# Optimization experiments

Hardware: AMD Instinct MI355X
Metric: run time of the kernel (lower is better)

## Reference

```python
import jax, jax.numpy as jnp
import numpy as np

NB_CLASSES = 10
EPS = 1e-8  # torch cosine_similarity eps


def gcn_conv(x, W, b, src, dst, n):
    h = x @ W
    deg = jax.ops.segment_sum(jnp.ones_like(src, dtype=h.dtype), dst, num_segments=n) + 1.0
    dinv = deg ** -0.5
    coef = (dinv[src] * dinv[dst])[:, None]
    agg = jax.ops.segment_sum(h[src] * coef, dst, num_segments=n)
    return agg + h * (1.0 / deg)[:, None] + b


def condition_net(e, w_in, b_in, w_hid, b_hid, w_out, b_out):
    # ConditionNet with num_layers=2: input_fc -> elu -> hidden_fc[0] -> elu -> output_fc
    h = jax.nn.elu(e @ w_in + b_in)
    h = jax.nn.elu(h @ w_hid + b_hid)
    return h @ w_out + b_out


def setup_inputs() -> dict:
    key = jax.random.key(0)
    N, E, D, H, T, M = 20000, 320000, 256, 256, 3, 2048
    ks = jax.random.split(key, 24)
    s = 1.0 / np.sqrt(D)
    inp = {
        "x": jax.random.normal(ks[0], (N, D), dtype=jnp.float32),
        "src": jax.random.randint(ks[1], (E,), 0, N, dtype=jnp.int32),
        "dst": jax.random.randint(ks[2], (E,), 0, N, dtype=jnp.int32),
        "idx": jax.random.randint(ks[3], (M,), 0, N, dtype=jnp.int32),
        "labels": jax.random.randint(ks[4], (M,), 0, NB_CLASSES, dtype=jnp.int32),
        "train": 1,
        # 3 GCNConv layers (all D->D, residual structure forces equal widths)
        "gcn_W1": jax.random.normal(ks[5], (D, D), dtype=jnp.float32) * s,
        "gcn_b1": jnp.zeros((D,), dtype=jnp.float32),
        "gcn_W2": jax.random.normal(ks[6], (D, D), dtype=jnp.float32) * s,
        "gcn_b2": jnp.zeros((D,), dtype=jnp.float32),
        "gcn_W3": jax.random.normal(ks[7], (D, D), dtype=jnp.float32) * s,
        "gcn_b3": jnp.zeros((D,), dtype=jnp.float32),
        # T=3 ConditionNets, params stacked on leading axis
        "cn_w_in": jax.random.normal(ks[8], (T, D, H), dtype=jnp.float32) * s,
        "cn_b_in": jnp.zeros((T, H), dtype=jnp.float32),
        "cn_w_hid": jax.random.normal(ks[9], (T, H, H), dtype=jnp.float32) * s,
        "cn_b_hid": jnp.zeros((T, H), dtype=jnp.float32),
        "cn_w_out": jax.random.normal(ks[10], (T, H, D), dtype=jnp.float32) * s,
        "cn_b_out": jnp.zeros((T, D), dtype=jnp.float32),
        # Embed_prompt
        "p_list": jax.random.normal(ks[11], (5, D), dtype=jnp.float32) * s,
        "a_W": jax.random.normal(ks[12], (D, 5), dtype=jnp.float32) * s,
        "a_b": jnp.zeros((5,), dtype=jnp.float32),
        # gcn_weight2 (trainable); weight1 and weight3 are frozen zeros, closed over
        "gcn_weight2": jnp.float32(1.0),
    }
    return inp


def reference(x, src, dst, idx, labels, train,
              gcn_W1, gcn_b1, gcn_W2, gcn_b2, gcn_W3, gcn_b3,
              cn_w_in, cn_b_in, cn_w_hid, cn_b_hid, cn_w_out, cn_b_out,
              p_list, a_W, a_b, gcn_weight2):
    n = x.shape[0]
    origin_x = x
    w1 = jnp.float32(0.0)  # gcn_weight1 (frozen)
    w3 = jnp.float32(0.0)  # gcn_weight3 (frozen)
    T = cn_w_in.shape[0]
    for t in range(T):  # think layers (small static count)
        e1 = gcn_conv(x, gcn_W1, gcn_b1, src, dst, n)
        e2 = gcn_conv(e1, gcn_W2, gcn_b2, src, dst, n) + e1
        e3 = gcn_conv(e2, gcn_W3, gcn_b3, src, dst, n) + e2
        embed = w1 * e1 + gcn_weight2 * e2 + w3 * e3
        prompt = condition_net(embed, cn_w_in[t], cn_b_in[t], cn_w_hid[t], cn_b_hid[t],
                               cn_w_out[t], cn_b_out[t])
        x = prompt * origin_x
    # full gcn(x, edge_index): 3 convs with ELU activation (standard GCN forward)
    h = jax.nn.elu(gcn_conv(x, gcn_W1, gcn_b1, src, dst, n))
    h = jax.nn.elu(gcn_conv(h, gcn_W2, gcn_b2, src, dst, n))
    h = jax.nn.elu(gcn_conv(h, gcn_W3, gcn_b3, src, dst, n))
    # Embed_prompt: attention over 5 learned prompt vectors
    weight = jax.nn.softmax(h @ a_W + a_b, axis=1)  # [N, 5]
    embed = h + weight @ p_list
    rawret = embed[idx]  # [M, D]
    # train==1: class prototypes via scatter-mean over labels
    sums = jax.ops.segment_sum(rawret, labels, num_segments=NB_CLASSES)
    counts = jax.ops.segment_sum(jnp.ones_like(labels, dtype=rawret.dtype), labels,
                                 num_segments=NB_CLASSES)
    ave = sums / jnp.maximum(counts, 1.0)[:, None]  # [C, D]
    # fused cosine similarity: normalize both, one matmul (replaces M*C scalar loop)
    rn = rawret / jnp.maximum(jnp.linalg.norm(rawret, axis=1, keepdims=True), EPS)
    an = ave / jnp.maximum(jnp.linalg.norm(ave, axis=1, keepdims=True), EPS)
    ret = jax.nn.softmax(rn @ an.T, axis=1)  # [M, C]
    return ret
```

## Files before the change

kernel.cpp:

```cpp
#include <hip/hip_runtime.h>
#include <hip/hip_bf16.h>
#include <math.h>

#define NN 20000
#define DD 256
#define EE 320000
#define MM 2048
#define CC 10
#define TT 3

typedef __attribute__((ext_vector_type(8))) short s8v;
typedef __attribute__((ext_vector_type(4))) float f4v;

__device__ unsigned short g_xb[NN * DD];
__device__ unsigned short g_xo[NN * DD];
__device__ unsigned short g_hb[NN * DD];
__device__ unsigned short g_e1b[NN * DD];
__device__ unsigned short g_e2b[NN * DD];
__device__ int   g_cnt[NN];
__device__ int   g_cursor[NN];
__device__ int   g_rowstart[NN + 1];
__device__ float g_dinv[NN];
__device__ float g_invdeg[NN];
__device__ int   g_part[128];
__device__ int2  g_edge[EE];
__device__ float g_sums[CC * DD];
__device__ float g_cntf[CC];
__device__ unsigned short g_wT1[12 * DD * DD];
__device__ unsigned short g_wT2[12 * DD * DD];

__device__ __forceinline__ float wave_sum(float v) {
#pragma unroll
  for (int off = 32; off > 0; off >>= 1) v += __shfl_xor(v, off);
  return v;
}

__device__ __forceinline__ float eluf(float x) {
  return x > 0.f ? x : expm1f(x);
}

__device__ __forceinline__ float2 bfpair(unsigned int d) {
  union { unsigned int i; float f; } a, b;
  a.i = d << 16;
  b.i = d & 0xffff0000u;
  return make_float2(a.f, b.f);
}

__device__ __forceinline__ unsigned int packbf(float x, float y) {
  union { __hip_bfloat162 v; unsigned int u; } c;
  c.v = __float22bfloat162_rn(make_float2(x, y));
  return c.u;
}

__device__ __forceinline__ void gl_lds16(const unsigned short* g, unsigned short* l) {
  __builtin_amdgcn_global_load_lds(
      (const __attribute__((address_space(1))) unsigned int*)g,
      (__attribute__((address_space(3))) unsigned int*)l, 16, 0, 0);
}

struct WPtrs { const float* p[12]; };

__global__ __launch_bounds__(256) void init_k(const float* __restrict__ x,
                                              unsigned short* __restrict__ xb,
                                              WPtrs wp) {
  __shared__ float t[64][65];
  int b = blockIdx.x;
  int tid = threadIdx.x;
  if (b < 2500) {
    int i = b * 256 + tid;
    const float4* x4 = (const float4*)x;
    float4 a = x4[i * 2], bb = x4[i * 2 + 1];
    uint4 o;
    o.x = packbf(a.x, a.y);
    o.y = packbf(a.z, a.w);
    o.z = packbf(bb.x, bb.y);
    o.w = packbf(bb.z, bb.w);
    ((uint4*)xb)[i] = o;
  } else if (b < 2692) {
    int bb = b - 2500;
    int widx = bb >> 4;
    int rem = bb & 15;
    int kt0 = (rem >> 2) * 64, nt0 = (rem & 3) * 64;
    const float* W = wp.p[widx];
    int ln = tid & 63, lk = tid >> 6;
    for (int kk = lk; kk < 64; kk += 4)
      t[kk][ln] = W[(size_t)(kt0 + kk) * DD + nt0 + ln];
    __syncthreads();
    for (int nn = lk; nn < 64; nn += 4) {
      float v = t[ln][nn];
      __hip_bfloat16 hb = __float2bfloat16(v);
      float hf = __bfloat162float(hb);
      __hip_bfloat16 lb = __float2bfloat16(v - hf);
      union { __hip_bfloat16 b; unsigned short s; } ch, cl;
      ch.b = hb; cl.b = lb;
      size_t o = (size_t)widx * DD * DD + (size_t)(nt0 + nn) * DD + kt0 + ln;
      g_wT1[o] = ch.s;
      g_wT2[o] = cl.s;
    }
  } else {
    int i = (b - 2692) * 256 + tid;
    if (i < NN) { g_cnt[i] = 0; g_cursor[i] = 0; }
    if (i < CC * DD) g_sums[i] = 0.f;
    if (i < CC) g_cntf[i] = 0.f;
  }
}

__global__ void hist_k(const int* __restrict__ dst) {
  int e = blockIdx.x * blockDim.x + threadIdx.x;
  if (e < EE) atomicAdd(&g_cnt[dst[e]], 1);
}

__global__ __launch_bounds__(256) void scanA_k() {
  __shared__ int s[256];
  int t = threadIdx.x;
  int i = blockIdx.x * 256 + t;
  int v = (i < NN) ? g_cnt[i] : 0;
  s[t] = v;
  __syncthreads();
#pragma unroll
  for (int off = 128; off > 0; off >>= 1) {
    if (t < off) s[t] += s[t + off];
    __syncthreads();
  }
  if (t == 0) g_part[blockIdx.x] = s[0];
}

__global__ __launch_bounds__(256) void scanC_k() {
  __shared__ int ps[128];
  __shared__ int s[256];
  int t = threadIdx.x;
  if (t < 128) ps[t] = (t < 79) ? g_part[t] : 0;
  __syncthreads();
#pragma unroll
  for (int off = 1; off < 128; off <<= 1) {
    int v = (t >= off && t < 128) ? ps[t - off] : 0;
    __syncthreads();
    if (t < 128) ps[t] += v;
    __syncthreads();
  }
  int base = (blockIdx.x == 0) ? 0 : ps[blockIdx.x - 1];
  int i = blockIdx.x * 256 + t;
  int v = (i < NN) ? g_cnt[i] : 0;
  s[t] = v;
  __syncthreads();
#pragma unroll
  for (int off = 1; off < 256; off <<= 1) {
    int x2 = (t >= off) ? s[t - off] : 0;
    __syncthreads();
    s[t] += x2;
    __syncthreads();
  }
  if (i < NN) {
    g_rowstart[i] = base + s[t] - v;
    float dg = (float)(v + 1);
    g_invdeg[i] = 1.0f / dg;
    g_dinv[i] = 1.0f / sqrtf(dg);
  }
  if (blockIdx.x == 78 && t == 0) g_rowstart[NN] = EE;
}

__global__ void fill_k(const int* __restrict__ src, const int* __restrict__ dst) {
  int e = blockIdx.x * blockDim.x + threadIdx.x;
  if (e < EE) {
    int d = dst[e];
    int p = atomicAdd(&g_cursor[d], 1);
    int j = g_rowstart[d] + p;
    int si = src[e];
    float coef = g_dinv[si] * g_dinv[d];
    g_edge[j] = make_int2(si * 512, __float_as_int(coef));
  }
}

template <int SPLIT>
union GemmSM {
  unsigned short st[2][(1024 + 512 * SPLIT) * 8];
  float ct[64][68];
};

template <int EPI, int SPLIT>
__global__ __launch_bounds__(256) void gemm_k(const unsigned short* __restrict__ A,
                                              const unsigned short* __restrict__ B1,
                                              const unsigned short* __restrict__ B2,
                                              unsigned short* __restrict__ C,
                                              const float* __restrict__ bias,
                                              const float* __restrict__ alphap,
                                              const unsigned short* __restrict__ mul) {
  __shared__ GemmSM<SPLIT> sm;
  constexpr int CB = 1024 + 512 * SPLIT;
  int b = blockIdx.x;
  int xcd = b & 7, off = b >> 3;
  int logical = (xcd < 4) ? xcd * 157 + off : 628 + (xcd - 4) * 156 + off;
  int mblk = logical >> 2, nblk = logical & 3;
  int row0 = mblk * 64, col0 = nblk * 64;

  int tid = threadIdx.x;
  int wv = tid >> 6, lane = tid & 63;
  int wm = wv >> 1, wn = wv & 1;
  int lr = lane & 15, lk = lane >> 4;

  f4v acc[2][2];
#pragma unroll
  for (int i = 0; i < 2; ++i)
#pragma unroll
    for (int j = 0; j < 2; ++j) acc[i][j] = (f4v){0.f, 0.f, 0.f, 0.f};

  auto stage = [&](int buf, int kt) {
    unsigned short* base = sm.st[buf];
#pragma unroll
    for (int i = 0; i < CB / 256; ++i) {
      int cb = (wv * (CB / 256) + i) * 64;
      int c = cb + lane;
      unsigned short* ldst = base + (size_t)cb * 8;
      if (c < 512) {
        int row = c >> 3, pos = c & 7;
        int kc = pos ^ (row & 7);
        int gr = row0 + row;
        gr = gr < NN ? gr : NN - 1;
        gl_lds16(A + (size_t)gr * DD + kt + kc * 8, ldst);
      } else if (c < 1024) {
        int c2 = c - 512;
        int col = c2 >> 3, pos = c2 & 7;
        int kc = pos ^ (col & 7);
        gl_lds16(B1 + (size_t)(col0 + col) * DD + kt + kc * 8, ldst);
      } else {
        int c2 = c - 1024;
        int col = c2 >> 3, pos = c2 & 7;
        int kc = pos ^ (col & 7);
        gl_lds16(B2 + (size_t)(col0 + col) * DD + kt + kc * 8, ldst);
      }
    }
  };

  stage(0, 0);
  __syncthreads();

  int buf = 0;
#pragma unroll
  for (int t = 0; t < 4; ++t) {
    if (t < 3) stage(buf ^ 1, (t + 1) * 64);
    const unsigned short* base = sm.st[buf];
#pragma unroll
    for (int ksub = 0; ksub < 2; ++ksub) {
      int kc = ksub * 4 + lk;
      s8v a[2], b1v[2], b2v[2];
#pragma unroll
      for (int mi = 0; mi < 2; ++mi) {
        int row = wm * 32 + mi * 16 + lr;
        a[mi] = *(const s8v*)(base + (row * 8 + (kc ^ (row & 7))) * 8);
      }
#pragma unroll
      for (int nj = 0; nj < 2; ++nj) {
        int col = wn * 32 + nj * 16 + lr;
        int ch = col * 8 + (kc ^ (col & 7));
        b1v[nj] = *(const s8v*)(base + (512 + ch) * 8);
        if (SPLIT) b2v[nj] = *(const s8v*)(base + (1024 + ch) * 8);
      }
#pragma unroll
      for (int mi = 0; mi < 2; ++mi)
#pragma unroll
        for (int nj = 0; nj < 2; ++nj) {
          acc[mi][nj] = __builtin_amdgcn_mfma_f32_16x16x32_bf16(a[mi], b1v[nj], acc[mi][nj], 0, 0, 0);
          if (SPLIT)
            acc[mi][nj] = __builtin_amdgcn_mfma_f32_16x16x32_bf16(a[mi], b2v[nj], acc[mi][nj], 0, 0, 0);
        }
    }
    __syncthreads();
    buf ^= 1;
  }

#pragma unroll
  for (int mi = 0; mi < 2; ++mi)
#pragma unroll
    for (int nj = 0; nj < 2; ++nj)
#pragma unroll
      for (int r = 0; r < 4; ++r)
        sm.ct[wm * 32 + mi * 16 + lk * 4 + r][wn * 32 + nj * 16 + lr] = acc[mi][nj][r];
  __syncthreads();

  float alpha = 1.f;
  if (EPI == 1) alpha = alphap ? *alphap : 1.f;
#pragma unroll
  for (int p = 0; p < 2; ++p) {
    int row = p * 32 + (tid >> 3);
    int c0 = (tid & 7) * 8;
    int gr = row0 + row;
    int gc = col0 + c0;
    if (gr < NN) {
      float v[8];
      float4 va = *(float4*)&sm.ct[row][c0];
      float4 vb = *(float4*)&sm.ct[row][c0 + 4];
      v[0] = va.x; v[1] = va.y; v[2] = va.z; v[3] = va.w;
      v[4] = vb.x; v[5] = vb.y; v[6] = vb.z; v[7] = vb.w;
      if (EPI == 1) {
        float4 bv0 = *(const float4*)(bias + gc);
        float4 bv1 = *(const float4*)(bias + gc + 4);
        float bb[8] = {bv0.x, bv0.y, bv0.z, bv0.w, bv1.x, bv1.y, bv1.z, bv1.w};
#pragma unroll
        for (int i = 0; i < 8; ++i) v[i] = eluf(fmaf(alpha, v[i], bb[i]));
      } else if (EPI == 2) {
        float4 bv0 = *(const float4*)(bias + gc);
        float4 bv1 = *(const float4*)(bias + gc + 4);
        float bb[8] = {bv0.x, bv0.y, bv0.z, bv0.w, bv1.x, bv1.y, bv1.z, bv1.w};
        uint4 mu = *(const uint4*)(mul + (size_t)gr * DD + gc);
        float2 m0 = bfpair(mu.x), m1 = bfpair(mu.y), m2 = bfpair(mu.z), m3 = bfpair(mu.w);
        float mm[8] = {m0.x, m0.y, m1.x, m1.y, m2.x, m2.y, m3.x, m3.y};
#pragma unroll
        for (int i = 0; i < 8; ++i) v[i] = (v[i] + bb[i]) * mm[i];
      }
      uint4 o;
      o.x = packbf(v[0], v[1]);
      o.y = packbf(v[2], v[3]);
      o.z = packbf(v[4], v[5]);
      o.w = packbf(v[6], v[7]);
      *(uint4*)(C + (size_t)gr * DD + gc) = o;
    }
  }
}

template <int RES>
__device__ __forceinline__ void agg_row8(int row, int sl, int hf,
                                         const unsigned short* __restrict__ h,
                                         const float* __restrict__ bias,
                                         const unsigned short* __restrict__ res,
                                         float* o) {
  const char* hb = (const char*)h;
  int lo = sl * 16;
  float acc[8];
#pragma unroll
  for (int k = 0; k < 8; ++k) acc[k] = 0.f;
  int s = g_rowstart[row], e = g_rowstart[row + 1];
  int j = s;
  for (; j + 12 <= e; j += 12) {
    int2 E[6];
    uint4 V[6];
#pragma unroll
    for (int u = 0; u < 6; ++u) E[u] = g_edge[j + 2 * u + hf];
#pragma unroll
    for (int u = 0; u < 6; ++u) V[u] = *(const uint4*)(hb + (size_t)E[u].x + lo);
#pragma unroll
    for (int u = 0; u < 6; ++u) {
      float c = __int_as_float(E[u].y);
      float2 p0 = bfpair(V[u].x), p1 = bfpair(V[u].y);
      float2 p2 = bfpair(V[u].z), p3 = bfpair(V[u].w);
      acc[0] = fmaf(c, p0.x, acc[0]); acc[1] = fmaf(c, p0.y, acc[1]);
      acc[2] = fmaf(c, p1.x, acc[2]); acc[3] = fmaf(c, p1.y, acc[3]);
      acc[4] = fmaf(c, p2.x, acc[4]); acc[5] = fmaf(c, p2.y, acc[5]);
      acc[6] = fmaf(c, p3.x, acc[6]); acc[7] = fmaf(c, p3.y, acc[7]);
    }
  }
  if (j < e) {
    int2 E[6];
    uint4 V[6];
    int live[6];
#pragma unroll
    for (int u = 0; u < 6; ++u) {
      int jj = j + 2 * u + hf;
      live[u] = jj < e;
      E[u] = g_edge[live[u] ? jj : e - 1];
    }
#pragma unroll
    for (int u = 0; u < 6; ++u) V[u] = *(const uint4*)(hb + (size_t)E[u].x + lo);
#pragma unroll
    for (int u = 0; u < 6; ++u) {
      float c = live[u] ? __int_as_float(E[u].y) : 0.f;
      float2 p0 = bfpair(V[u].x), p1 = bfpair(V[u].y);
      float2 p2 = bfpair(V[u].z), p3 = bfpair(V[u].w);
      acc[0] = fmaf(c, p0.x, acc[0]); acc[1] = fmaf(c, p0.y, acc[1]);
      acc[2] = fmaf(c, p1.x, acc[2]); acc[3] = fmaf(c, p1.y, acc[3]);
      acc[4] = fmaf(c, p2.x, acc[4]); acc[5] = fmaf(c, p2.y, acc[5]);
      acc[6] = fmaf(c, p3.x, acc[6]); acc[7] = fmaf(c, p3.y, acc[7]);
    }
  }
#pragma unroll
  for (int k = 0; k < 8; ++k) acc[k] += __shfl_xor(acc[k], 32);
  float idg = g_invdeg[row];
  uint4 hv = *(const uint4*)(hb + (size_t)row * 512 + lo);
  float2 h0 = bfpair(hv.x), h1 = bfpair(hv.y), h2 = bfpair(hv.z), h3 = bfpair(hv.w);
  float hw[8] = {h0.x, h0.y, h1.x, h1.y, h2.x, h2.y, h3.x, h3.y};
  float4 b0 = *(const float4*)(bias + sl * 8);
  float4 b1 = *(const float4*)(bias + sl * 8 + 4);
  float bb[8] = {b0.x, b0.y, b0.z, b0.w, b1.x, b1.y, b1.z, b1.w};
#pragma unroll
  for (int k = 0; k < 8; ++k) o[k] = acc[k] + hw[k] * idg + bb[k];
  if (RES) {
    uint4 rv = *(const uint4*)((const char*)res + (size_t)row * 512 + lo);
    float2 r0 = bfpair(rv.x), r1 = bfpair(rv.y), r2 = bfpair(rv.z), r3 = bfpair(rv.w);
    float rw[8] = {r0.x, r0.y, r1.x, r1.y, r2.x, r2.y, r3.x, r3.y};
#pragma unroll
    for (int k = 0; k < 8; ++k) o[k] += rw[k];
  }
}

template <int ELU, int RES>
__global__ __launch_bounds__(256) void agg_k(const unsigned short* __restrict__ h,
                                             const float* __restrict__ bias,
                                             const unsigned short* __restrict__ res,
                                             unsigned short* __restrict__ out) {
  int row = (blockIdx.x * 256 + threadIdx.x) >> 6;
  int lane = threadIdx.x & 63;
  int sl = lane & 31, hf = lane >> 5;
  float o[8];
  agg_row8<RES>(row, sl, hf, h, bias, res, o);
  if (ELU) {
#pragma unroll
    for (int k = 0; k < 8; ++k) o[k] = eluf(o[k]);
  }
  if (hf == 0) {
    uint4 pk;
    pk.x = packbf(o[0], o[1]);
    pk.y = packbf(o[2], o[3]);
    pk.z = packbf(o[4], o[5]);
    pk.w = packbf(o[6], o[7]);
    *(uint4*)((char*)out + (size_t)row * 512 + sl * 16) = pk;
  }
}

__global__ __launch_bounds__(256) void agg_idx_k(const unsigned short* __restrict__ h,
                                                 const float* __restrict__ bias,
                                                 const int* __restrict__ idxp,
                                                 unsigned short* __restrict__ gath) {
  int m = (blockIdx.x * 256 + threadIdx.x) >> 6;
  int lane = threadIdx.x & 63;
  int sl = lane & 31, hf = lane >> 5;
  int row = idxp[m];
  float o[8];
  agg_row8<0>(row, sl, hf, h, bias, nullptr, o);
#pragma unroll
  for (int k = 0; k < 8; ++k) o[k] = eluf(o[k]);
  if (hf == 0) {
    uint4 pk;
    pk.x = packbf(o[0], o[1]);
    pk.y = packbf(o[2], o[3]);
    pk.z = packbf(o[4], o[5]);
    pk.w = packbf(o[6], o[7]);
    *(uint4*)((char*)gath + (size_t)m * 512 + sl * 16) = pk;
  }
}

__device__ __forceinline__ float4 attn_apply(float4 r, int lane,
                                             const float* __restrict__ aW,
                                             const float* __restrict__ ab,
                                             const float* __restrict__ plist) {
  int d = lane * 4;
  float lg[5];
#pragma unroll
  for (int k = 0; k < 5; ++k) {
    float p = r.x * aW[(d + 0) * 5 + k] + r.y * aW[(d + 1) * 5 + k] +
              r.z * aW[(d + 2) * 5 + k] + r.w * aW[(d + 3) * 5 + k];
    lg[k] = wave_sum(p) + ab[k];
  }
  float mx = lg[0];
#pragma unroll
  for (int k = 1; k < 5; ++k) mx = fmaxf(mx, lg[k]);
  float w[5], sum = 0.f;
#pragma unroll
  for (int k = 0; k < 5; ++k) { w[k] = expf(lg[k] - mx); sum += w[k]; }
  float inv = 1.f / sum;
#pragma unroll
  for (int k = 0; k < 5; ++k) {
    float wk = w[k] * inv;
    float4 pv = *(const float4*)(plist + k * DD + d);
    r.x = fmaf(wk, pv.x, r.x);
    r.y = fmaf(wk, pv.y, r.y);
    r.z = fmaf(wk, pv.z, r.z);
    r.w = fmaf(wk, pv.w, r.w);
  }
  return r;
}

__global__ __launch_bounds__(256) void proto_k(const unsigned short* __restrict__ gath,
                                               const int* __restrict__ labels,
                                               const float* __restrict__ aW,
                                               const float* __restrict__ ab,
                                               const float* __restrict__ plist) {
  __shared__ float sums[CC][DD];
  __shared__ float cnts[CC];
  int t = threadIdx.x;
#pragma unroll
  for (int c = 0; c < CC; ++c) sums[c][t] = 0.f;
  if (t < CC) cnts[t] = 0.f;
  __syncthreads();
  int wv = t >> 6, lane = t & 63;
  int m0 = blockIdx.x * 64 + wv * 16;
  int d = lane * 4;
  for (int rr = 0; rr < 16; ++rr) {
    int m = m0 + rr;
    int lab = labels[m];
    uint2 rv = *(const uint2*)((const char*)gath + (size_t)m * 512 + lane * 8);
    float2 a0 = bfpair(rv.x), a1 = bfpair(rv.y);
    float4 r = attn_apply(make_float4(a0.x, a0.y, a1.x, a1.y), lane, aW, ab, plist);
    atomicAdd(&sums[lab][d + 0], r.x);
    atomicAdd(&sums[lab][d + 1], r.y);
    atomicAdd(&sums[lab][d + 2], r.z);
    atomicAdd(&sums[lab][d + 3], r.w);
    if (lane == 0) atomicAdd(&cnts[lab], 1.f);
  }
  __syncthreads();
#pragma unroll
  for (int c = 0; c < CC; ++c) atomicAdd(&g_sums[c * DD + t], sums[c][t]);
  if (t < CC) atomicAdd(&g_cntf[t], cnts[t]);
}

__global__ __launch_bounds__(256) void cos_k(const unsigned short* __restrict__ gath,
                                             const float* __restrict__ aW,
                                             const float* __restrict__ ab,
                                             const float* __restrict__ plist,
                                             float* __restrict__ out) {
  __shared__ float an[CC][DD];
  __shared__ float red[4];
  int t = threadIdx.x;
  int lane = t & 63, wv = t >> 6;
  for (int c = 0; c < CC; ++c) {
    float v = g_sums[c * DD + t] / fmaxf(g_cntf[c], 1.0f);
    float sq = wave_sum(v * v);
    if (lane == 0) red[wv] = sq;
    __syncthreads();
    float tot = red[0] + red[1] + red[2] + red[3];
    float nrm = fmaxf(sqrtf(tot), 1e-8f);
    an[c][t] = v / nrm;
    __syncthreads();
  }
  int wid = (blockIdx.x * 256 + t) >> 6;
  if (wid >= MM) return;
  uint2 rv = *(const uint2*)((const char*)gath + (size_t)wid * 512 + lane * 8);
  float2 r0 = bfpair(rv.x), r1 = bfpair(rv.y);
  float4 r = attn_apply(make_float4(r0.x, r0.y, r1.x, r1.y), lane, aW, ab, plist);
  float n = wave_sum(r.x * r.x + r.y * r.y + r.z * r.z + r.w * r.w);
  float rnf = 1.0f / fmaxf(sqrtf(n), 1e-8f);
  float lg[CC];
#pragma unroll
  for (int c = 0; c < CC; ++c) {
    float4 a = ((const float4*)&an[c][0])[lane];
    float p = r.x * a.x + r.y * a.y + r.z * a.z + r.w * a.w;
    lg[c] = wave_sum(p) * rnf;
  }
  float mx = lg[0];
#pragma unroll
  for (int c = 1; c < CC; ++c) mx = fmaxf(mx, lg[c]);
  float s = 0.f, w[CC];
#pragma unroll
  for (int c = 0; c < CC; ++c) { w[c] = expf(lg[c] - mx); s += w[c]; }
  float inv = 1.f / s;
#pragma unroll
  for (int c = 0; c < CC; ++c)
    if (lane == c) out[(size_t)wid * CC + c] = w[c] * inv;
}

extern "C" void kernel_launch(void* const* d_in, const int* in_sizes, int n_in,
                              void* d_out, int out_size, void* d_ws, size_t ws_size,
                              hipStream_t stream) {
  (void)in_sizes; (void)n_in; (void)d_ws; (void)ws_size; (void)out_size;
  const float* x      = (const float*)d_in[0];
  const int*   src    = (const int*)d_in[1];
  const int*   dst    = (const int*)d_in[2];
  const int*   idx    = (const int*)d_in[3];
  const int*   labels = (const int*)d_in[4];
  const float* W1 = (const float*)d_in[6];
  const float* b1 = (const float*)d_in[7];
  const float* W2 = (const float*)d_in[8];
  const float* b2 = (const float*)d_in[9];
  const float* W3 = (const float*)d_in[10];
  const float* b3 = (const float*)d_in[11];
  const float* cw_in  = (const float*)d_in[12];
  const float* cb_in  = (const float*)d_in[13];
  const float* cw_hid = (const float*)d_in[14];
  const float* cb_hid = (const float*)d_in[15];
  const float* cw_out = (const float*)d_in[16];
  const float* cb_out = (const float*)d_in[17];
  const float* plist  = (const float*)d_in[18];
  const float* aW     = (const float*)d_in[19];
  const float* ab     = (const float*)d_in[20];
  const float* w2s    = (const float*)d_in[21];
  float* out = (float*)d_out;

  unsigned short *xb, *xo, *hb, *e1b, *e2b, *wt1, *wt2;
  hipGetSymbolAddress((void**)&xb,  HIP_SYMBOL(g_xb));
  hipGetSymbolAddress((void**)&xo,  HIP_SYMBOL(g_xo));
  hipGetSymbolAddress((void**)&hb,  HIP_SYMBOL(g_hb));
  hipGetSymbolAddress((void**)&e1b, HIP_SYMBOL(g_e1b));
  hipGetSymbolAddress((void**)&e2b, HIP_SYMBOL(g_e2b));
  hipGetSymbolAddress((void**)&wt1, HIP_SYMBOL(g_wT1));
  hipGetSymbolAddress((void**)&wt2, HIP_SYMBOL(g_wT2));

  auto WT1 = [&](int w) { return (const unsigned short*)(wt1 + (size_t)w * DD * DD); };
  auto WT2 = [&](int w) { return (const unsigned short*)(wt2 + (size_t)w * DD * DD); };

  WPtrs wp;
  wp.p[0] = W1; wp.p[1] = W2; wp.p[2] = W3;
  for (int t = 0; t < 3; ++t) {
    wp.p[3 + t] = cw_in  + (size_t)t * DD * DD;
    wp.p[6 + t] = cw_hid + (size_t)t * DD * DD;
    wp.p[9 + t] = cw_out + (size_t)t * DD * DD;
  }
  init_k<<<2771, 256, 0, stream>>>(x, xb, wp);
  hist_k<<<1250, 256, 0, stream>>>(dst);
  scanA_k<<<79, 256, 0, stream>>>();
  scanC_k<<<79, 256, 0, stream>>>();
  fill_k<<<1250, 256, 0, stream>>>(src, dst);

  const int GG = 1252;
  const unsigned short* xin = xb;
  for (int t = 0; t < TT; ++t) {
    gemm_k<0, 1><<<GG, 256, 0, stream>>>(xin, WT1(0), WT2(0), hb, nullptr, nullptr, nullptr);
    agg_k<0, 0><<<5000, 256, 0, stream>>>(hb, b1, nullptr, e1b);
    gemm_k<0, 1><<<GG, 256, 0, stream>>>(e1b, WT1(1), WT2(1), hb, nullptr, nullptr, nullptr);
    agg_k<0, 1><<<5000, 256, 0, stream>>>(hb, b2, e1b, e2b);
    gemm_k<1, 0><<<GG, 256, 0, stream>>>(e2b, WT1(3 + t), WT1(3 + t), e1b,
                                         cb_in + (size_t)t * DD, w2s, nullptr);
    gemm_k<1, 0><<<GG, 256, 0, stream>>>(e1b, WT1(6 + t), WT1(6 + t), hb,
                                         cb_hid + (size_t)t * DD, nullptr, nullptr);
    gemm_k<2, 0><<<GG, 256, 0, stream>>>(hb, WT1(9 + t), WT1(9 + t), xo,
                                         cb_out + (size_t)t * DD, nullptr, xb);
    xin = xo;
  }

  gemm_k<0, 1><<<GG, 256, 0, stream>>>(xin, WT1(0), WT2(0), hb, nullptr, nullptr, nullptr);
  agg_k<1, 0><<<5000, 256, 0, stream>>>(hb, b1, nullptr, e1b);
  gemm_k<0, 1><<<GG, 256, 0, stream>>>(e1b, WT1(1), WT2(1), hb, nullptr, nullptr, nullptr);
  agg_k<1, 0><<<5000, 256, 0, stream>>>(hb, b2, nullptr, e2b);
  gemm_k<0, 1><<<GG, 256, 0, stream>>>(e2b, WT1(2), WT2(2), hb, nullptr, nullptr, nullptr);
  agg_idx_k<<<512, 256, 0, stream>>>(hb, b3, idx, e1b);

  proto_k<<<32, 256, 0, stream>>>(e1b, labels, aW, ab, plist);
  cos_k<<<512, 256, 0, stream>>>(e1b, aW, ab, plist, out);
}
```

Baseline: 556.5 us.

## Drop split-bf16 GCN weights, preload full B tile, merge scan kernels

The GCN layer GEMMs previously used hi+lo bf16 weight splits and ran two MFMAs per tile. They now use a single bf16 weight copy, which halves MFMA work and B traffic for those GEMMs at the cost of weight precision. The GEMM also loads the full 64x256 B tile into LDS once up front, so only A is double-buffered. The two-kernel degree scan is merged into one kernel where each block recomputes the partition sums, removing a launch.

```diff
diff --git a/kernel.cpp b/kernel.cpp
--- a/kernel.cpp
+++ b/kernel.cpp
@@ -22,12 +22,10 @@
 __device__ int   g_rowstart[NN + 1];
 __device__ float g_dinv[NN];
 __device__ float g_invdeg[NN];
-__device__ int   g_part[128];
 __device__ int2  g_edge[EE];
 __device__ float g_sums[CC * DD];
 __device__ float g_cntf[CC];
 __device__ unsigned short g_wT1[12 * DD * DD];
-__device__ unsigned short g_wT2[12 * DD * DD];
 
 __device__ __forceinline__ float wave_sum(float v) {
 #pragma unroll
@@ -88,14 +86,9 @@
     __syncthreads();
     for (int nn = lk; nn < 64; nn += 4) {
       float v = t[ln][nn];
-      __hip_bfloat16 hb = __float2bfloat16(v);
-      float hf = __bfloat162float(hb);
-      __hip_bfloat16 lb = __float2bfloat16(v - hf);
-      union { __hip_bfloat16 b; unsigned short s; } ch, cl;
-      ch.b = hb; cl.b = lb;
-      size_t o = (size_t)widx * DD * DD + (size_t)(nt0 + nn) * DD + kt0 + ln;
-      g_wT1[o] = ch.s;
-      g_wT2[o] = cl.s;
+      union { __hip_bfloat16 b; unsigned short s; } ch;
+      ch.b = __float2bfloat16(v);
+      g_wT1[(size_t)widx * DD * DD + (size_t)(nt0 + nn) * DD + kt0 + ln] = ch.s;
     }
   } else {
     int i = (b - 2692) * 256 + tid;
@@ -110,26 +103,29 @@
   if (e < EE) atomicAdd(&g_cnt[dst[e]], 1);
 }
 
-__global__ __launch_bounds__(256) void scanA_k() {
-  __shared__ int s[256];
-  int t = threadIdx.x;
-  int i = blockIdx.x * 256 + t;
-  int v = (i < NN) ? g_cnt[i] : 0;
-  s[t] = v;
-  __syncthreads();
-#pragma unroll
-  for (int off = 128; off > 0; off >>= 1) {
-    if (t < off) s[t] += s[t + off];
-    __syncthreads();
-  }
-  if (t == 0) g_part[blockIdx.x] = s[0];
-}
-
-__global__ __launch_bounds__(256) void scanC_k() {
+__global__ __launch_bounds__(256) void scan_k() {
   __shared__ int ps[128];
   __shared__ int s[256];
   int t = threadIdx.x;
-  if (t < 128) ps[t] = (t < 79) ? g_part[t] : 0;
+  if (t < 128) ps[t] = 0;
+  __syncthreads();
+  if (t < 79) {
+    const uint4* c4 = (const uint4*)g_cnt;
+    int base4 = t * 64;
+    int sum = 0;
+    for (int i = 0; i < 64; ++i) {
+      int idx = base4 + i;
+      if (idx * 4 < NN) {
+        uint4 v = c4[idx];
+        int lim = NN - idx * 4;
+        sum += (int)v.x;
+        if (lim > 1) sum += (int)v.y;
+        if (lim > 2) sum += (int)v.z;
+        if (lim > 3) sum += (int)v.w;
+      }
+    }
+    ps[t] = sum;
+  }
   __syncthreads();
 #pragma unroll
   for (int off = 1; off < 128; off <<= 1) {
@@ -171,22 +167,19 @@
   }
 }
 
-template <int SPLIT>
 union GemmSM {
-  unsigned short st[2][(1024 + 512 * SPLIT) * 8];
+  struct { unsigned short A[2][512 * 8]; unsigned short B[2048 * 8]; } st;
   float ct[64][68];
 };
 
-template <int EPI, int SPLIT>
+template <int EPI>
 __global__ __launch_bounds__(256) void gemm_k(const unsigned short* __restrict__ A,
-                                              const unsigned short* __restrict__ B1,
-                                              const unsigned short* __restrict__ B2,
+                                              const unsigned short* __restrict__ B,
                                               unsigned short* __restrict__ C,
                                               const float* __restrict__ bias,
                                               const float* __restrict__ alphap,
                                               const unsigned short* __restrict__ mul) {
-  __shared__ GemmSM<SPLIT> sm;
-  constexpr int CB = 1024 + 512 * SPLIT;
+  __shared__ GemmSM sm;
   int b = blockIdx.x;
   int xcd = b & 7, off = b >> 3;
   int logical = (xcd < 4) ? xcd * 157 + off : 628 + (xcd - 4) * 156 + off;
@@ -204,65 +197,56 @@
 #pragma unroll
     for (int j = 0; j < 2; ++j) acc[i][j] = (f4v){0.f, 0.f, 0.f, 0.f};
 
-  auto stage = [&](int buf, int kt) {
-    unsigned short* base = sm.st[buf];
-#pragma unroll
-    for (int i = 0; i < CB / 256; ++i) {
-      int cb = (wv * (CB / 256) + i) * 64;
+#pragma unroll
+  for (int i = 0; i < 8; ++i) {
+    int cb = (wv * 8 + i) * 64;
+    int c = cb + lane;
+    int col = c >> 5, pos = c & 31;
+    int kc = pos ^ (col & 7);
+    gl_lds16(B + (size_t)(col0 + col) * DD + kc * 8, sm.st.B + (size_t)cb * 8);
+  }
+
+  auto stageA = [&](int buf, int kt) {
+#pragma unroll
+    for (int i = 0; i < 2; ++i) {
+      int cb = (wv * 2 + i) * 64;
       int c = cb + lane;
-      unsigned short* ldst = base + (size_t)cb * 8;
-      if (c < 512) {
-        int row = c >> 3, pos = c & 7;
-        int kc = pos ^ (row & 7);
-        int gr = row0 + row;
-        gr = gr < NN ? gr : NN - 1;
-        gl_lds16(A + (size_t)gr * DD + kt + kc * 8, ldst);
-      } else if (c < 1024) {
-        int c2 = c - 512;
-        int col = c2 >> 3, pos = c2 & 7;
-        int kc = pos ^ (col & 7);
-        gl_lds16(B1 + (size_t)(col0 + col) * DD + kt + kc * 8, ldst);
-      } else {
-        int c2 = c - 1024;
-        int col = c2 >> 3, pos = c2 & 7;
-        int kc = pos ^ (col & 7);
-        gl_lds16(B2 + (size_t)(col0 + col) * DD + kt + kc * 8, ldst);
-      }
+      int row = c >> 3, pos = c & 7;
+      int kc = pos ^ (row & 7);
+      int gr = row0 + row;
+      gr = gr < NN ? gr : NN - 1;
+      gl_lds16(A + (size_t)gr * DD + kt + kc * 8, sm.st.A[buf] + (size_t)cb * 8);
     }
   };
 
-  stage(0, 0);
+  stageA(0, 0);
   __syncthreads();
 
   int buf = 0;
 #pragma unroll
   for (int t = 0; t < 4; ++t) {
-    if (t < 3) stage(buf ^ 1, (t + 1) * 64);
-    const unsigned short* base = sm.st[buf];
+    if (t < 3) stageA(buf ^ 1, (t + 1) * 64);
+    const unsigned short* baseA = sm.st.A[buf];
 #pragma unroll
     for (int ksub = 0; ksub < 2; ++ksub) {
-      int kc = ksub * 4 + lk;
-      s8v a[2], b1v[2], b2v[2];
+      int kct = ksub * 4 + lk;
+      int kcg = t * 8 + kct;
+      s8v a[2], bv[2];
 #pragma unroll
       for (int mi = 0; mi < 2; ++mi) {
         int row = wm * 32 + mi * 16 + lr;
-        a[mi] = *(const s8v*)(base + (row * 8 + (kc ^ (row & 7))) * 8);
+        a[mi] = *(const s8v*)(baseA + (row * 8 + (kct ^ (row & 7))) * 8);
       }
 #pragma unroll
       for (int nj = 0; nj < 2; ++nj) {
         int col = wn * 32 + nj * 16 + lr;
-        int ch = col * 8 + (kc ^ (col & 7));
-        b1v[nj] = *(const s8v*)(base + (512 + ch) * 8);
-        if (SPLIT) b2v[nj] = *(const s8v*)(base + (1024 + ch) * 8);
+        bv[nj] = *(const s8v*)(sm.st.B + (col * 32 + (kcg ^ (col & 7))) * 8);
       }
 #pragma unroll
       for (int mi = 0; mi < 2; ++mi)
 #pragma unroll
-        for (int nj = 0; nj < 2; ++nj) {
-          acc[mi][nj] = __builtin_amdgcn_mfma_f32_16x16x32_bf16(a[mi], b1v[nj], acc[mi][nj], 0, 0, 0);
-          if (SPLIT)
-            acc[mi][nj] = __builtin_amdgcn_mfma_f32_16x16x32_bf16(a[mi], b2v[nj], acc[mi][nj], 0, 0, 0);
-        }
+        for (int nj = 0; nj < 2; ++nj)
+          acc[mi][nj] = __builtin_amdgcn_mfma_f32_16x16x32_bf16(a[mi], bv[nj], acc[mi][nj], 0, 0, 0);
     }
     __syncthreads();
     buf ^= 1;
@@ -573,17 +557,15 @@
   const float* w2s    = (const float*)d_in[21];
   float* out = (float*)d_out;
 
-  unsigned short *xb, *xo, *hb, *e1b, *e2b, *wt1, *wt2;
+  unsigned short *xb, *xo, *hb, *e1b, *e2b, *wt1;
   hipGetSymbolAddress((void**)&xb,  HIP_SYMBOL(g_xb));
   hipGetSymbolAddress((void**)&xo,  HIP_SYMBOL(g_xo));
   hipGetSymbolAddress((void**)&hb,  HIP_SYMBOL(g_hb));
   hipGetSymbolAddress((void**)&e1b, HIP_SYMBOL(g_e1b));
   hipGetSymbolAddress((void**)&e2b, HIP_SYMBOL(g_e2b));
   hipGetSymbolAddress((void**)&wt1, HIP_SYMBOL(g_wT1));
-  hipGetSymbolAddress((void**)&wt2, HIP_SYMBOL(g_wT2));
 
   auto WT1 = [&](int w) { return (const unsigned short*)(wt1 + (size_t)w * DD * DD); };
-  auto WT2 = [&](int w) { return (const unsigned short*)(wt2 + (size_t)w * DD * DD); };
 
   WPtrs wp;
   wp.p[0] = W1; wp.p[1] = W2; wp.p[2] = W3;
@@ -594,31 +576,30 @@
   }
   init_k<<<2771, 256, 0, stream>>>(x, xb, wp);
   hist_k<<<1250, 256, 0, stream>>>(dst);
-  scanA_k<<<79, 256, 0, stream>>>();
-  scanC_k<<<79, 256, 0, stream>>>();
+  scan_k<<<79, 256, 0, stream>>>();
   fill_k<<<1250, 256, 0, stream>>>(src, dst);
 
   const int GG = 1252;
   const unsigned short* xin = xb;
   for (int t = 0; t < TT; ++t) {
-    gemm_k<0, 1><<<GG, 256, 0, stream>>>(xin, WT1(0), WT2(0), hb, nullptr, nullptr, nullptr);
+    gemm_k<0><<<GG, 256, 0, stream>>>(xin, WT1(0), hb, nullptr, nullptr, nullptr);
     agg_k<0, 0><<<5000, 256, 0, stream>>>(hb, b1, nullptr, e1b);
-    gemm_k<0, 1><<<GG, 256, 0, stream>>>(e1b, WT1(1), WT2(1), hb, nullptr, nullptr, nullptr);
+    gemm_k<0><<<GG, 256, 0, stream>>>(e1b, WT1(1), hb, nullptr, nullptr, nullptr);
     agg_k<0, 1><<<5000, 256, 0, stream>>>(hb, b2, e1b, e2b);
-    gemm_k<1, 0><<<GG, 256, 0, stream>>>(e2b, WT1(3 + t), WT1(3 + t), e1b,
-                                         cb_in + (size_t)t * DD, w2s, nullptr);
-    gemm_k<1, 0><<<GG, 256, 0, stream>>>(e1b, WT1(6 + t), WT1(6 + t), hb,
-                                         cb_hid + (size_t)t * DD, nullptr, nullptr);
-    gemm_k<2, 0><<<GG, 256, 0, stream>>>(hb, WT1(9 + t), WT1(9 + t), xo,
-                                         cb_out + (size_t)t * DD, nullptr, xb);
+    gemm_k<1><<<GG, 256, 0, stream>>>(e2b, WT1(3 + t), e1b,
+                                      cb_in + (size_t)t * DD, w2s, nullptr);
+    gemm_k<1><<<GG, 256, 0, stream>>>(e1b, WT1(6 + t), hb,
+                                      cb_hid + (size_t)t * DD, nullptr, nullptr);
+    gemm_k<2><<<GG, 256, 0, stream>>>(hb, WT1(9 + t), xo,
+                                      cb_out + (size_t)t * DD, nullptr, xb);
     xin = xo;
   }
 
-  gemm_k<0, 1><<<GG, 256, 0, stream>>>(xin, WT1(0), WT2(0), hb, nullptr, nullptr, nullptr);
+  gemm_k<0><<<GG, 256, 0, stream>>>(xin, WT1(0), hb, nullptr, nullptr, nullptr);
   agg_k<1, 0><<<5000, 256, 0, stream>>>(hb, b1, nullptr, e1b);
-  gemm_k<0, 1><<<GG, 256, 0, stream>>>(e1b, WT1(1), WT2(1), hb, nullptr, nullptr, nullptr);
+  gemm_k<0><<<GG, 256, 0, stream>>>(e1b, WT1(1), hb, nullptr, nullptr, nullptr);
   agg_k<1, 0><<<5000, 256, 0, stream>>>(hb, b2, nullptr, e2b);
-  gemm_k<0, 1><<<GG, 256, 0, stream>>>(e2b, WT1(2), WT2(2), hb, nullptr, nullptr, nullptr);
+  gemm_k<0><<<GG, 256, 0, stream>>>(e2b, WT1(2), hb, nullptr, nullptr, nullptr);
   agg_idx_k<<<512, 256, 0, stream>>>(hb, b3, idx, e1b);
 
   proto_k<<<32, 256, 0, stream>>>(e1b, labels, aW, ab, plist);
```

Measured after the change: 574.8 us. 3.3% more time.
